# Optimization experiments

Measured on AMD Instinct MI355X. Metric: run time of the kernel, lower is better.

## Reference

```python
import jax, jax.numpy as jnp
import numpy as np

FORGET_BIAS = 1.0


def setup_inputs() -> dict:
    key = jax.random.key(0)
    k1, k2, k3, k4 = jax.random.split(key, 4)
    B, T, D, H, C = 512, 128, 256, 256, 128
    x = jax.random.normal(k1, (B, T, D), dtype=jnp.float32)
    # BasicLSTMCell fused kernel: [(D + H), 4*H], gates ordered (i, j, f, o)
    kernel = jax.random.normal(k2, (D + H, 4 * H), dtype=jnp.float32) * 0.05
    bias = jnp.zeros((4 * H,), dtype=jnp.float32)
    w_out = jax.random.normal(k3, (H, C), dtype=jnp.float32) * 0.05
    b_out = jnp.zeros((C,), dtype=jnp.float32)
    return {"x": x, "kernel": kernel, "bias": bias, "w_out": w_out, "b_out": b_out}


def reference(x, kernel, bias, w_out, b_out):
    B, T, D = x.shape
    H = w_out.shape[0]
    x = x.astype(jnp.float32)

    def step(carry, xt):
        c, h = carry
        z = jnp.concatenate([xt, h], axis=-1) @ kernel + bias  # [B, 4H]
        i, j, f, o = jnp.split(z, 4, axis=-1)
        new_c = c * jax.nn.sigmoid(f + FORGET_BIAS) + jax.nn.sigmoid(i) * jnp.tanh(j)
        new_h = jnp.tanh(new_c) * jax.nn.sigmoid(o)
        return (new_c, new_h), new_h

    c0 = jnp.zeros((B, H), dtype=jnp.float32)
    h0 = jnp.zeros((B, H), dtype=jnp.float32)
    xs = jnp.swapaxes(x, 0, 1)  # [T, B, D] -- unstack along time axis 1
    (_, h_last), _ = jax.lax.scan(step, (c0, h0), xs)
    return h_last @ w_out + b_out
```

## Files before the change

kernel.cpp:

```cpp
#include <hip/hip_runtime.h>
#include <hip/hip_fp16.h>
#include <stdint.h>
#include <stddef.h>


typedef __attribute__((ext_vector_type(8))) __bf16 bf16x8;
typedef __attribute__((ext_vector_type(4))) __bf16 bf16x4;
typedef __attribute__((ext_vector_type(4))) float  f32x4;
typedef __attribute__((ext_vector_type(8))) int    i32x8;

#define LDH   264
#define LDF   272
#define ZPS   2097152ull
#define SONE  0x7F7F7F7F

__device__ __forceinline__ f32x4 mfma_bf16(bf16x8 a, bf16x8 b, f32x4 c) {
    return __builtin_amdgcn_mfma_f32_16x16x32_bf16(a, b, c, 0, 0, 0);
}
#define EXP2(x) __builtin_amdgcn_exp2f(x)
#define RCP(x)  __builtin_amdgcn_rcpf(x)
#define L2E  1.442695040f
#define L2E2 2.885390082f

__global__ __launch_bounds__(256) void shuffle_w(const float* __restrict__ Wk,
                                                 __bf16* __restrict__ WxF,
                                                 unsigned char* __restrict__ WhF) {
    int id = blockIdx.x * 256 + threadIdx.x;
    if (id < 32768) {
        int lane = id & 63, kt = (id >> 6) & 7, nt = id >> 9;
        int quad = lane >> 4, l16 = lane & 15;
        const float* src = Wk + (size_t)(kt * 32 + quad * 8) * 1024 + nt * 16 + l16;
        __bf16* dst = WxF + ((size_t)(nt * 8 + kt) * 64 + lane) * 8;
#pragma unroll
        for (int j = 0; j < 8; ++j) dst[j] = (__bf16)src[(size_t)j * 1024];
    } else if (id < 40960) {
        int i = id - 32768;
        int lane = i & 63, kt = (i >> 6) & 1, ng = i >> 7;
        int n = ng * 16 + (lane & 15);
        int kb = 256 + kt * 128 + (lane >> 4) * 32;
        int* dst = (int*)(WhF + (((size_t)ng * 2 + kt) * 64 + lane) * 32);
#pragma unroll
        for (int d = 0; d < 8; ++d) {
            float w0 = Wk[(size_t)(kb + 4 * d + 0) * 1024 + n];
            float w1 = Wk[(size_t)(kb + 4 * d + 1) * 1024 + n];
            float w2 = Wk[(size_t)(kb + 4 * d + 2) * 1024 + n];
            float w3 = Wk[(size_t)(kb + 4 * d + 3) * 1024 + n];
            int lo = __builtin_amdgcn_cvt_pk_fp8_f32(w0, w1, 0, false);
            dst[d]  = __builtin_amdgcn_cvt_pk_fp8_f32(w2, w3, lo, true);
        }
    }
}

__global__ __launch_bounds__(512, 2) void xproj(const float* __restrict__ x,
        const __bf16* __restrict__ WxF, const float* __restrict__ bias,
        uint2* __restrict__ Zx) {
    __shared__ __attribute__((aligned(16))) __bf16 At[64 * LDH];
    const int tid = threadIdx.x, wv = tid >> 6, lane = tid & 63;
    const int l16 = lane & 15, quad = lane >> 4;
    const int rb = blockIdx.x & 31, tg = blockIdx.x >> 5;

#pragma unroll
    for (int rr = 0; rr < 8; ++rr) {
        int Arow = wv * 8 + rr;
        int tt = Arow >> 4, r = Arow & 15;
        const float4 xv = *((const float4*)(x + ((size_t)(rb * 16 + r) * 128 + tg * 4 + tt) * 256) + lane);
        bf16x4 xb = { (__bf16)xv.x, (__bf16)xv.y, (__bf16)xv.z, (__bf16)xv.w };
        *(bf16x4*)&At[Arow * LDH + lane * 4] = xb;
    }
    __syncthreads();

    f32x4 acc[4][8];
#pragma unroll
    for (int tt = 0; tt < 4; ++tt)
#pragma unroll
        for (int nt = 0; nt < 8; ++nt) acc[tt][nt] = (f32x4){0.f, 0.f, 0.f, 0.f};

#pragma unroll
    for (int kt = 0; kt < 8; ++kt) {
        bf16x8 af[4];
#pragma unroll
        for (int tt = 0; tt < 4; ++tt)
            af[tt] = *(const bf16x8*)&At[(tt * 16 + l16) * LDH + kt * 32 + quad * 8];
#pragma unroll
        for (int nt = 0; nt < 8; ++nt) {
            bf16x8 wf = *(const bf16x8*)&WxF[(((size_t)(wv * 8 + nt) * 8 + kt) * 64 + lane) * 8];
#pragma unroll
            for (int tt = 0; tt < 4; ++tt) acc[tt][nt] = mfma_bf16(af[tt], wf, acc[tt][nt]);
        }
    }

#pragma unroll
    for (int nt = 0; nt < 8; ++nt) {
        int col = wv * 128 + nt * 16 + l16;
        float bb = bias[col] + ((col >= 512 && col < 768) ? 1.0f : 0.0f);
#pragma unroll
        for (int tt = 0; tt < 4; ++tt) {
            int t = tg * 4 + tt;
            union { __half h[4]; uint2 u; } pk;
#pragma unroll
            for (int r = 0; r < 4; ++r) pk.h[r] = __float2half(acc[tt][nt][r] + bb);
            Zx[(size_t)wv * ZPS + ((size_t)(rb * 128 + t) * 8 + nt) * 64 + lane] = pk.u;
        }
    }
}

#define LSTM_STEP(TT, ZR, ZZU, ZRE, ZZE, RBUF, WBUF)                           \
    {                                                                          \
        i32x8 afr[2];                                                          \
        _Pragma("unroll")                                                      \
        for (int kt = 0; kt < 2; ++kt) {                                       \
            const uint4* ap = (const uint4*)&HtF[RBUF][l16 * LDF + kt * 128 + quad * 32]; \
            uint4 lo = ap[0], hi = ap[1];                                      \
            afr[kt] = (i32x8){(int)lo.x, (int)lo.y, (int)lo.z, (int)lo.w,      \
                              (int)hi.x, (int)hi.y, (int)hi.z, (int)hi.w};     \
        }                                                                      \
        f32x4 acc[8];                                                          \
        _Pragma("unroll")                                                      \
        for (int p = 0; p < 8; ++p) acc[p] = (f32x4){ZZU[p], 0.f, 0.f, 0.f};   \
        {                                                                      \
            int tl = ((TT) + 2 > 127) ? 127 : ((TT) + 2);                      \
            size_t zi = zi0 + (size_t)tl * 512;                                \
            _Pragma("unroll")                                                  \
            for (int p = 0; p < 8; ++p) ZR[p] = Zx[p * ZPS + zi];              \
        }                                                                      \
        __builtin_amdgcn_s_setprio(1);                                         \
        _Pragma("unroll")                                                      \
        for (int kt = 0; kt < 2; ++kt)                                         \
            _Pragma("unroll")                                                  \
            for (int p = 0; p < 8; ++p)                                        \
                acc[p] = __builtin_amdgcn_mfma_scale_f32_16x16x128_f8f6f4(     \
                    afr[kt], wreg[p * 2 + kt], acc[p], 0, 0, 0, SONE, 0, SONE);\
        __builtin_amdgcn_s_setprio(0);                                         \
        _Pragma("unroll")                                                      \
        for (int p = 0; p < 8; ++p) {                                          \
            unsigned w = (quad & 2) ? ZRE[p].y : ZRE[p].x;                     \
            w = (quad & 1) ? (w >> 16) : (w & 0xffff);                         \
            union { unsigned short u; __half h; } cv; cv.u = (unsigned short)w;\
            ZZE[p] = __half2float(cv.h);                                       \
        }                                                                      \
        unsigned char* ldsw = &HtF[WBUF][0];                                   \
        _Pragma("unroll")                                                      \
        for (int hf = 0; hf < 2; ++hf) {                                       \
            float iv = acc[0 + hf][0];                                         \
            float jv = acc[2 + hf][0];                                         \
            float fv = acc[4 + hf][0];                                         \
            float ov = acc[6 + hf][0];                                         \
            float si = RCP(1.f + EXP2(-L2E * iv));                             \
            float sf = RCP(1.f + EXP2(-L2E * fv));                             \
            float so = RCP(1.f + EXP2(-L2E * ov));                             \
            float tj = 2.f * RCP(1.f + EXP2(-L2E2 * jv)) - 1.f;                \
            float c = c_[hf] * sf + si * tj;                                   \
            c_[hf] = c;                                                        \
            float tc = 2.f * RCP(1.f + EXP2(-L2E2 * c)) - 1.f;                 \
            float h = tc * so;                                                 \
            hr[hf] = h;                                                        \
            unsigned pb = (unsigned)__builtin_amdgcn_cvt_pk_fp8_f32(h, h, 0, false); \
            ldsw[(4 * quad) * LDF + hf * 128 + col0] = (unsigned char)pb;      \
        }                                                                      \
        __syncthreads();           \
    }

__global__ __launch_bounds__(512, 2) void lstm_rec(const unsigned char* __restrict__ WhF,
        const uint2* __restrict__ Zx, const float* __restrict__ wout,
        const float* __restrict__ bout, float* __restrict__ out) {
    __shared__ __attribute__((aligned(16))) unsigned char HtF[2][16 * LDF];
    __shared__ __attribute__((aligned(16))) __bf16 HtB[16 * LDH];
    const int tid = threadIdx.x, wv = tid >> 6, lane = tid & 63;
    const int l16 = lane & 15, quad = lane >> 4;
    const int rbblk = blockIdx.x;
    const int rb = rbblk >> 2, qb = rbblk & 3;

    i32x8 wreg[16];
#pragma unroll
    for (int p = 0; p < 8; ++p) {
        int ng = (p >> 1) * 16 + (p & 1) * 8 + wv;
#pragma unroll
        for (int kt = 0; kt < 2; ++kt) {
            const uint4* wp = (const uint4*)(WhF + (((size_t)ng * 2 + kt) * 64 + lane) * 32);
            uint4 lo = wp[0], hi = wp[1];
            wreg[p * 2 + kt] = (i32x8){(int)lo.x, (int)lo.y, (int)lo.z, (int)lo.w,
                                       (int)hi.x, (int)hi.y, (int)hi.z, (int)hi.w};
        }
    }
    for (int i = tid; i < (16 * LDF * 2) / 4; i += 512) ((uint*)HtF[0])[i] = 0u;

    const int col0 = wv * 16 + l16;
    float c_[2] = {0.f, 0.f};
    float hr[2] = {0.f, 0.f};
    const size_t zi0 = ((size_t)rb * 1024 + wv) * 64 + qb * 16 + l16;

    uint2 zrA[8], zrB[8];
    float zzA[8], zzB[8];
#pragma unroll
    for (int p = 0; p < 8; ++p) zrA[p] = Zx[p * ZPS + zi0];
#pragma unroll
    for (int p = 0; p < 8; ++p) zrB[p] = Zx[p * ZPS + zi0 + 512];
#pragma unroll
    for (int p = 0; p < 8; ++p) {
        unsigned w = (quad & 2) ? zrA[p].y : zrA[p].x;
        w = (quad & 1) ? (w >> 16) : (w & 0xffff);
        union { unsigned short u; __half h; } cv; cv.u = (unsigned short)w;
        zzA[p] = __half2float(cv.h);
    }
    __syncthreads();

#pragma unroll 1
    for (int t = 0; t < 128; t += 2) {
        LSTM_STEP(t,     zrA, zzA, zrB, zzB, 0, 1);
        LSTM_STEP(t + 1, zrB, zzB, zrA, zzA, 1, 0);
    }

    for (int i = tid; i < 16 * LDH; i += 512) HtB[i] = (__bf16)0.f;
    __syncthreads();
#pragma unroll
    for (int hf = 0; hf < 2; ++hf)
        HtB[(4 * quad) * LDH + hf * 128 + col0] = (__bf16)hr[hf];
    __syncthreads();

    bf16x8 wo[8];
#pragma unroll
    for (int kt = 0; kt < 8; ++kt) {
        bf16x8 f;
#pragma unroll
        for (int j = 0; j < 8; ++j)
            f[j] = (__bf16)wout[(size_t)(kt * 32 + quad * 8 + j) * 128 + col0];
        wo[kt] = f;
    }
    f32x4 oa = {0.f, 0.f, 0.f, 0.f};
#pragma unroll
    for (int kt = 0; kt < 8; ++kt) {
        bf16x8 af = *(const bf16x8*)&HtB[l16 * LDH + kt * 32 + quad * 8];
        oa = mfma_bf16(af, wo[kt], oa);
    }
    out[(size_t)(rbblk * 4 + quad) * 128 + col0] = oa[0] + bout[col0];
}

extern "C" void kernel_launch(void* const* d_in, const int* in_sizes, int n_in,
                              void* d_out, int out_size, void* d_ws, size_t ws_size,
                              hipStream_t stream) {
    const float* x    = (const float*)d_in[0];
    const float* Wk   = (const float*)d_in[1];
    const float* bias = (const float*)d_in[2];
    const float* wout = (const float*)d_in[3];
    const float* bout = (const float*)d_in[4];
    float* out = (float*)d_out;

    __bf16*        WxF = (__bf16*)d_ws;
    unsigned char* WhF = (unsigned char*)d_ws + 524288;
    uint2*         Zx  = (uint2*)((char*)d_ws + 2097152);

    shuffle_w<<<160, 256, 0, stream>>>(Wk, WxF, WhF);
    xproj<<<1024, 512, 0, stream>>>(x, WxF, bias, Zx);
    lstm_rec<<<128, 512, 0, stream>>>(WhF, Zx, wout, bout, out);
}
```

Before: 413.7 us.

## Retile xproj into smaller column-split blocks with double-buffered K-slab staging

The input projection kernel is restructured so each block handles 128 rows (16 batch x 8 timesteps) by one 128-column gate slice. The K dimension is streamed in 32-wide slabs through double-buffered shared memory, and the global load of the next slab overlaps the current MFMAs. Instead of 1024 blocks of 512 threads it launches 4096 blocks of 256, with a 2x2 warp tiling. This aims to raise occupancy and hide load latency. The cost is that x is re-read 8 times, once per column slice, and a barrier is added per K step.

New measurement: 432.6 us. 4.6% more time.

```diff
diff --git a/kernel.cpp b/kernel.cpp
--- a/kernel.cpp
+++ b/kernel.cpp
@@ -13,6 +13,7 @@
 #define LDF   272
 #define ZPS   2097152ull
 #define SONE  0x7F7F7F7F
+#define LDA   36
 
 __device__ __forceinline__ f32x4 mfma_bf16(bf16x8 a, bf16x8 b, f32x4 c) {
     return __builtin_amdgcn_mfma_f32_16x16x32_bf16(a, b, c, 0, 0, 0);
@@ -51,55 +52,81 @@
     }
 }
 
-__global__ __launch_bounds__(512, 2) void xproj(const float* __restrict__ x,
+__global__ __launch_bounds__(256, 2) void xproj(const float* __restrict__ x,
         const __bf16* __restrict__ WxF, const float* __restrict__ bias,
         uint2* __restrict__ Zx) {
-    __shared__ __attribute__((aligned(16))) __bf16 At[64 * LDH];
-    const int tid = threadIdx.x, wv = tid >> 6, lane = tid & 63;
-    const int l16 = lane & 15, quad = lane >> 4;
-    const int rb = blockIdx.x & 31, tg = blockIdx.x >> 5;
-
-#pragma unroll
-    for (int rr = 0; rr < 8; ++rr) {
-        int Arow = wv * 8 + rr;
-        int tt = Arow >> 4, r = Arow & 15;
-        const float4 xv = *((const float4*)(x + ((size_t)(rb * 16 + r) * 128 + tg * 4 + tt) * 256) + lane);
-        bf16x4 xb = { (__bf16)xv.x, (__bf16)xv.y, (__bf16)xv.z, (__bf16)xv.w };
-        *(bf16x4*)&At[Arow * LDH + lane * 4] = xb;
-    }
-    __syncthreads();
-
-    f32x4 acc[4][8];
+    __shared__ __attribute__((aligned(16))) __bf16 As[2][128 * LDA];
+    const int tid = threadIdx.x, w = tid >> 6, lane = tid & 63;
+    const int l16 = lane & 15, q = lane >> 4;
+    const int p = blockIdx.x & 7, bt = blockIdx.x >> 3;
+    const int bb = bt & 31, tg = bt >> 5;
+    const int wm = w >> 1, wn = w & 1;
+
+    {
+#pragma unroll
+        for (int i = 0; i < 4; ++i) {
+            int s = tid + i * 256, row = s >> 3, f4 = s & 7;
+            int b = bb * 16 + (row & 15), t_ = tg * 8 + (row >> 4);
+            float4 v = *((const float4*)(x + (size_t)(b * 128 + t_) * 256) + f4);
+            bf16x4 c4 = {(__bf16)v.x, (__bf16)v.y, (__bf16)v.z, (__bf16)v.w};
+            *(bf16x4*)&As[0][row * LDA + f4 * 4] = c4;
+        }
+    }
+    __syncthreads();
+
+    f32x4 acc[4][4];
 #pragma unroll
     for (int tt = 0; tt < 4; ++tt)
 #pragma unroll
-        for (int nt = 0; nt < 8; ++nt) acc[tt][nt] = (f32x4){0.f, 0.f, 0.f, 0.f};
-
-#pragma unroll
-    for (int kt = 0; kt < 8; ++kt) {
-        bf16x8 af[4];
-#pragma unroll
-        for (int tt = 0; tt < 4; ++tt)
-            af[tt] = *(const bf16x8*)&At[(tt * 16 + l16) * LDH + kt * 32 + quad * 8];
-#pragma unroll
-        for (int nt = 0; nt < 8; ++nt) {
-            bf16x8 wf = *(const bf16x8*)&WxF[(((size_t)(wv * 8 + nt) * 8 + kt) * 64 + lane) * 8];
-#pragma unroll
-            for (int tt = 0; tt < 4; ++tt) acc[tt][nt] = mfma_bf16(af[tt], wf, acc[tt][nt]);
-        }
-    }
-
-#pragma unroll
-    for (int nt = 0; nt < 8; ++nt) {
-        int col = wv * 128 + nt * 16 + l16;
-        float bb = bias[col] + ((col >= 512 && col < 768) ? 1.0f : 0.0f);
+        for (int nf = 0; nf < 4; ++nf) acc[tt][nf] = (f32x4){0.f, 0.f, 0.f, 0.f};
+
+#pragma unroll
+    for (int ks = 0; ks < 8; ++ks) {
+        float4 nv[4];
+        if (ks < 7) {
+#pragma unroll
+            for (int i = 0; i < 4; ++i) {
+                int s = tid + i * 256, row = s >> 3, f4 = s & 7;
+                int b = bb * 16 + (row & 15), t_ = tg * 8 + (row >> 4);
+                nv[i] = *((const float4*)(x + (size_t)(b * 128 + t_) * 256 + (size_t)(ks + 1) * 32) + f4);
+            }
+        }
+        bf16x8 wf[4];
+#pragma unroll
+        for (int nf = 0; nf < 4; ++nf) {
+            int ntF = p * 8 + wn * 4 + nf;
+            wf[nf] = *(const bf16x8*)&WxF[(((size_t)ntF * 8 + ks) * 64 + lane) * 8];
+        }
 #pragma unroll
         for (int tt = 0; tt < 4; ++tt) {
-            int t = tg * 4 + tt;
+            bf16x8 af = *(const bf16x8*)&As[ks & 1][(wm * 64 + tt * 16 + l16) * LDA + q * 8];
+#pragma unroll
+            for (int nf = 0; nf < 4; ++nf)
+                acc[tt][nf] = mfma_bf16(af, wf[nf], acc[tt][nf]);
+        }
+        if (ks < 7) {
+#pragma unroll
+            for (int i = 0; i < 4; ++i) {
+                int s = tid + i * 256, row = s >> 3, f4 = s & 7;
+                bf16x4 c4 = {(__bf16)nv[i].x, (__bf16)nv[i].y, (__bf16)nv[i].z, (__bf16)nv[i].w};
+                *(bf16x4*)&As[(ks + 1) & 1][row * LDA + f4 * 4] = c4;
+            }
+            __syncthreads();
+        }
+    }
+
+    const float fb = (p == 4 || p == 5) ? 1.0f : 0.0f;
+#pragma unroll
+    for (int nf = 0; nf < 4; ++nf) {
+        int cnt = wn * 4 + nf;
+        float bb_ = bias[p * 128 + cnt * 16 + l16] + fb;
+#pragma unroll
+        for (int tt = 0; tt < 4; ++tt) {
+            int t_ = tg * 8 + wm * 4 + tt;
             union { __half h[4]; uint2 u; } pk;
 #pragma unroll
-            for (int r = 0; r < 4; ++r) pk.h[r] = __float2half(acc[tt][nt][r] + bb);
-            Zx[(size_t)wv * ZPS + ((size_t)(rb * 128 + t) * 8 + nt) * 64 + lane] = pk.u;
+            for (int r = 0; r < 4; ++r) pk.h[r] = __float2half(acc[tt][nf][r] + bb_);
+            Zx[(size_t)p * ZPS + ((size_t)(bb * 128 + t_) * 8 + cnt) * 64 + q * 16 + l16] = pk.u;
         }
     }
 }
@@ -250,6 +277,6 @@
     uint2*         Zx  = (uint2*)((char*)d_ws + 2097152);
 
     shuffle_w<<<160, 256, 0, stream>>>(Wk, WxF, WhF);
-    xproj<<<1024, 512, 0, stream>>>(x, WxF, bias, Zx);
+    xproj<<<4096, 256, 0, stream>>>(x, WxF, bias, Zx);
     lstm_rec<<<128, 512, 0, stream>>>(WhF, Zx, wout, bout, out);
 }
```
